# Kernel optimization log

Hardware: AMD Instinct MI355X
Metric: run time of the kernel (lower is better)

## Reference

```python
import jax, jax.numpy as jnp
import numpy as np

B, T, E, H = 8, 2048, 1024, 64

def setup_inputs() -> dict:
    key = jax.random.key(0)
    kx, kq, kk, kv = jax.random.split(key, 4)
    x = jax.random.normal(kx, (B, T, E), dtype=jnp.float32)
    # torch Linear(E, H, bias=False): weight [H, E]; store transposed [E, H]
    scale = 1.0 / np.sqrt(E)
    Wq = jax.random.uniform(kq, (E, H), dtype=jnp.float32, minval=-scale, maxval=scale)
    Wk = jax.random.uniform(kk, (E, H), dtype=jnp.float32, minval=-scale, maxval=scale)
    Wv = jax.random.uniform(kv, (E, H), dtype=jnp.float32, minval=-scale, maxval=scale)
    return {"x": x, "Wq": Wq, "Wk": Wk, "Wv": Wv}

def reference(x, Wq, Wk, Wv):
    # x: [B,T,E]
    q = x @ Wq  # [B,T,H]
    k = x @ Wk
    v = x @ Wv
    head_size = q.shape[-1]
    scores = jnp.einsum('bth,bsh->bts', q, k) * (head_size ** -0.5)  # [B,T,T]
    Tlen = x.shape[1]
    causal = jnp.tril(jnp.ones((Tlen, Tlen), dtype=bool))
    scores = jnp.where(causal, scores, -jnp.inf)
    weights = jax.nn.softmax(scores, axis=-1)
    # dropout p=0.0 -> identity
    out = jnp.einsum('bts,bsh->bth', weights, v)  # [B,T,H]
    return out
```

## Files before the change

kernel.cpp:

```cpp
#include <hip/hip_runtime.h>
#include <hip/hip_bf16.h>

#define B_  8
#define T_  2048
#define E_  1024
#define H_  64
#define BT_ (B_*T_)

typedef __attribute__((ext_vector_type(8))) __bf16 bf16x8;
typedef __attribute__((ext_vector_type(4))) float  f32x4;

__device__ __forceinline__ unsigned short f2bfu(float f) {
    union { float f; unsigned u; } v; v.f = f;
    unsigned r = v.u + 0x7fffu + ((v.u >> 16) & 1u);
    return (unsigned short)(r >> 16);
}

__device__ __forceinline__ unsigned pk2(float lo, float hi) {
    __hip_bfloat162 h = __float22bfloat162_rn(float2{lo, hi});
    union { __hip_bfloat162 h; unsigned u; } v; v.h = h;
    return v.u;
}

#define QSCALE (0.125f * 1.44269504f)

__global__ __launch_bounds__(256)
void wprep_kernel(const float* __restrict__ Wq,
                  const float* __restrict__ Wk,
                  const float* __restrict__ Wv,
                  unsigned short* __restrict__ wf)
{
    const int c = blockIdx.x / 3;
    const int m = blockIdx.x % 3;
    const float* W = (m == 0) ? Wq : (m == 1 ? Wk : Wv);
    const float scale = (m == 0) ? QSCALE : 1.0f;

    const int n    = threadIdx.x >> 6;
    const int lane = threadIdx.x & 63;
    const int quad = lane >> 4;
    const int col  = lane & 15;
    const int h    = n * 16 + col;

    unsigned short tmp[8];
#pragma unroll
    for (int j = 0; j < 8; ++j)
        tmp[j] = f2bfu(W[(c * 32 + quad * 8 + j) * H_ + h] * scale);
    *(uint4*)&wf[(((c * 3 + m) * 4 + n) * 64 + lane) * 8] = *(uint4*)tmp;
}

__global__ __launch_bounds__(256, 4)
void qkv_kernel(const float* __restrict__ x,
                const unsigned short* __restrict__ wf,
                unsigned short* __restrict__ qb,
                unsigned short* __restrict__ kb,
                unsigned short* __restrict__ vtb)
{
    const int tid  = threadIdx.x;
    const int wave = tid >> 6;
    const int lane = tid & 63;
    const int quad = lane >> 4;
    const int col  = lane & 15;
    const long r0  = (long)blockIdx.x * 16;

    f32x4 acc[3];
#pragma unroll
    for (int m = 0; m < 3; ++m) acc[m] = (f32x4){0.f, 0.f, 0.f, 0.f};

    const float* xb = x + (r0 + col) * E_ + quad * 8;

    float4 ax[4][2];
#pragma unroll
    for (int d = 0; d < 4; ++d) {
        ax[d][0] = *(const float4*)(xb + d * 32);
        ax[d][1] = *(const float4*)(xb + d * 32 + 4);
    }
    bf16x8 bw[2][3];
#pragma unroll
    for (int d = 0; d < 2; ++d)
#pragma unroll
        for (int m = 0; m < 3; ++m)
            bw[d][m] = *(const bf16x8*)&wf[(((d * 3 + m) * 4 + wave) * 64 + lane) * 8];

    for (int c = 0; c < 32; ++c) {
        float4 a0 = ax[c & 3][0], a1 = ax[c & 3][1];
        bf16x8 b0 = bw[c & 1][0], b1 = bw[c & 1][1], b2 = bw[c & 1][2];

        if (c + 4 < 32) {
            ax[c & 3][0] = *(const float4*)(xb + (c + 4) * 32);
            ax[c & 3][1] = *(const float4*)(xb + (c + 4) * 32 + 4);
        }
        if (c + 2 < 32) {
#pragma unroll
            for (int m = 0; m < 3; ++m)
                bw[c & 1][m] = *(const bf16x8*)&wf[((((c + 2) * 3 + m) * 4 + wave) * 64 + lane) * 8];
        }

        unsigned pk[4];
        pk[0] = pk2(a0.x, a0.y);
        pk[1] = pk2(a0.z, a0.w);
        pk[2] = pk2(a1.x, a1.y);
        pk[3] = pk2(a1.z, a1.w);
        bf16x8 af = *(bf16x8*)pk;

        acc[0] = __builtin_amdgcn_mfma_f32_16x16x32_bf16(af, b0, acc[0], 0, 0, 0);
        acc[1] = __builtin_amdgcn_mfma_f32_16x16x32_bf16(af, b1, acc[1], 0, 0, 0);
        acc[2] = __builtin_amdgcn_mfma_f32_16x16x32_bf16(af, b2, acc[2], 0, 0, 0);
    }

    const int bidx = (int)(r0 >> 11);
    const int h    = wave * 16 + col;
#pragma unroll
    for (int r = 0; r < 4; ++r) {
        long t = r0 + quad * 4 + r;
        qb[t * H_ + h] = f2bfu(acc[0][r]);
        kb[t * H_ + h] = f2bfu(acc[1][r]);
        vtb[((long)(bidx * H_ + h)) * T_ + (t & (T_ - 1))] = f2bfu(acc[2][r]);
    }
}

#define PSS 72

__global__ __launch_bounds__(512, 2)
void attn_kernel(const unsigned short* __restrict__ qb,
                 const unsigned short* __restrict__ kb,
                 const unsigned short* __restrict__ vtb,
                 float* __restrict__ out)
{
    __shared__ char smem[8 * 16 * 68 * 4 + 8 * 2 * 16 * 4];
    unsigned short* ps = (unsigned short*)smem;
    float* oc = (float*)smem;
    float* ml = (float*)(smem + 8 * 16 * 68 * 4);

    const int tid  = threadIdx.x;
    const int g    = tid >> 6;
    const int lane = tid & 63;
    const int quad = lane >> 4;
    const int col  = lane & 15;
    const int b    = blockIdx.x & 7;
    const int p    = blockIdx.x >> 3;

    const unsigned short* qbb = qb  + (long)b * T_ * H_;
    const unsigned short* kbb = kb  + (long)b * T_ * H_;
    const unsigned short* vbb = vtb + (long)b * H_ * T_;

    for (int half = 0; half < 2; ++half) {
        const int qt = half ? (127 - p) : p;
        const int nt = (qt + 4) >> 2;

        bf16x8 qa0 = *(const bf16x8*)&qbb[(qt * 16 + col) * H_ + quad * 8];
        bf16x8 qa1 = *(const bf16x8*)&qbb[(qt * 16 + col) * H_ + 32 + quad * 8];

        f32x4 o[4];
        float m_i[4], l_i[4];
#pragma unroll
        for (int n = 0; n < 4; ++n) o[n] = (f32x4){0.f, 0.f, 0.f, 0.f};
#pragma unroll
        for (int r = 0; r < 4; ++r) { m_i[r] = -1e30f; l_i[r] = 0.f; }

        bf16x8 kf[8];
        if (g < nt) {
#pragma unroll
            for (int kt = 0; kt < 4; ++kt) {
                const unsigned short* kp = kbb + ((long)(g * 64 + kt * 16 + col)) * H_ + quad * 8;
                kf[kt * 2]     = *(const bf16x8*)kp;
                kf[kt * 2 + 1] = *(const bf16x8*)(kp + 32);
            }
        }

        for (int s = g; s < nt; s += 8) {
            f32x4 sa[4];
#pragma unroll
            for (int kt = 0; kt < 4; ++kt) {
                sa[kt] = (f32x4){0.f, 0.f, 0.f, 0.f};
                sa[kt] = __builtin_amdgcn_mfma_f32_16x16x32_bf16(qa0, kf[kt * 2],     sa[kt], 0, 0, 0);
                sa[kt] = __builtin_amdgcn_mfma_f32_16x16x32_bf16(qa1, kf[kt * 2 + 1], sa[kt], 0, 0, 0);
            }

            if (s + 8 < nt) {
#pragma unroll
                for (int kt = 0; kt < 4; ++kt) {
                    const unsigned short* kp = kbb + ((long)((s + 8) * 64 + kt * 16 + col)) * H_ + quad * 8;
                    kf[kt * 2]     = *(const bf16x8*)kp;
                    kf[kt * 2 + 1] = *(const bf16x8*)(kp + 32);
                }
            }

            if (s == nt - 1) {
#pragma unroll
                for (int kt = 0; kt < 4; ++kt) {
                    int kg = s * 64 + kt * 16 + col;
#pragma unroll
                    for (int r = 0; r < 4; ++r) {
                        int qg = qt * 16 + quad * 4 + r;
                        if (kg > qg) sa[kt][r] = -1e30f;
                    }
                }
            }

            float mx[4];
#pragma unroll
            for (int r = 0; r < 4; ++r)
                mx[r] = fmaxf(fmaxf(sa[0][r], sa[1][r]), fmaxf(sa[2][r], sa[3][r]));
#pragma unroll
            for (int off = 1; off < 16; off <<= 1)
#pragma unroll
                for (int r = 0; r < 4; ++r)
                    mx[r] = fmaxf(mx[r], __shfl_xor(mx[r], off, 64));

            float alpha[4], mnew[4];
#pragma unroll
            for (int r = 0; r < 4; ++r) {
                mnew[r]  = fmaxf(m_i[r], mx[r]);
                alpha[r] = __builtin_amdgcn_exp2f(m_i[r] - mnew[r]);
                m_i[r]   = mnew[r];
            }

            float rs[4] = {0.f, 0.f, 0.f, 0.f};
#pragma unroll
            for (int kt = 0; kt < 4; ++kt)
#pragma unroll
                for (int r = 0; r < 4; ++r) {
                    float pv = __builtin_amdgcn_exp2f(sa[kt][r] - mnew[r]);
                    rs[r] += pv;
                    ps[g * 16 * PSS + (quad * 4 + r) * PSS + kt * 16 + col] = f2bfu(pv);
                }
#pragma unroll
            for (int off = 1; off < 16; off <<= 1)
#pragma unroll
                for (int r = 0; r < 4; ++r)
                    rs[r] += __shfl_xor(rs[r], off, 64);
#pragma unroll
            for (int r = 0; r < 4; ++r)
                l_i[r] = l_i[r] * alpha[r] + rs[r];

#pragma unroll
            for (int n = 0; n < 4; ++n)
#pragma unroll
                for (int r = 0; r < 4; ++r)
                    o[n][r] *= alpha[r];

            bf16x8 pa0 = *(const bf16x8*)&ps[g * 16 * PSS + col * PSS + quad * 8];
            bf16x8 pa1 = *(const bf16x8*)&ps[g * 16 * PSS + col * PSS + 32 + quad * 8];
#pragma unroll
            for (int n = 0; n < 4; ++n) {
                const unsigned short* vp = vbb + ((long)(n * 16 + col)) * T_ + s * 64 + quad * 8;
                bf16x8 vf0 = *(const bf16x8*)vp;
                bf16x8 vf1 = *(const bf16x8*)(vp + 32);
                o[n] = __builtin_amdgcn_mfma_f32_16x16x32_bf16(pa0, vf0, o[n], 0, 0, 0);
                o[n] = __builtin_amdgcn_mfma_f32_16x16x32_bf16(pa1, vf1, o[n], 0, 0, 0);
            }
        }

        __syncthreads();
#pragma unroll
        for (int r = 0; r < 4; ++r) {
            int row = quad * 4 + r;
#pragma unroll
            for (int n = 0; n < 4; ++n)
                oc[(g * 16 + row) * 68 + n * 16 + col] = o[n][r];
        }
        if (col == 0) {
#pragma unroll
            for (int r = 0; r < 4; ++r) {
                ml[(g * 2 + 0) * 16 + quad * 4 + r] = m_i[r];
                ml[(g * 2 + 1) * 16 + quad * 4 + r] = l_i[r];
            }
        }
        __syncthreads();

#pragma unroll
        for (int rr = 0; rr < 2; ++rr) {
            int row = g * 2 + rr;
            float M = ml[0 * 32 + row];
#pragma unroll
            for (int j = 1; j < 8; ++j) M = fmaxf(M, ml[j * 32 + row]);
            float lsum = 0.f, osum = 0.f;
#pragma unroll
            for (int j = 0; j < 8; ++j) {
                float wgt = __builtin_amdgcn_exp2f(ml[j * 32 + row] - M);
                lsum += ml[j * 32 + 16 + row] * wgt;
                osum += oc[(j * 16 + row) * 68 + lane] * wgt;
            }
            out[((long)b * T_ + qt * 16 + row) * H_ + lane] = osum / lsum;
        }
        __syncthreads();
    }
}

extern "C" void kernel_launch(void* const* d_in, const int* in_sizes, int n_in,
                              void* d_out, int out_size, void* d_ws, size_t ws_size,
                              hipStream_t stream) {
    (void)in_sizes; (void)n_in; (void)out_size; (void)ws_size;
    const float* x  = (const float*)d_in[0];
    const float* Wq = (const float*)d_in[1];
    const float* Wk = (const float*)d_in[2];
    const float* Wv = (const float*)d_in[3];

    unsigned short* qb  = (unsigned short*)d_ws;
    unsigned short* kb  = qb + (size_t)BT_ * H_;
    unsigned short* vtb = kb + (size_t)BT_ * H_;
    unsigned short* wf  = vtb + (size_t)BT_ * H_;

    wprep_kernel<<<96, 256, 0, stream>>>(Wq, Wk, Wv, wf);
    qkv_kernel<<<BT_ / 16, 256, 0, stream>>>(x, wf, qb, kb, vtb);
    attn_kernel<<<B_ * 64, 512, 0, stream>>>(qb, kb, vtb, (float*)d_out);
}
```

Before: 170.1 us.

## Stage QKV weights and x tiles in LDS and prefetch V tiles early

The QKV projection kernel now stages each chunk of packed weights in double-buffered shared memory, using global_load_lds DMA when the builtin is available. The x tile is converted to bf16 cooperatively into LDS, so each global element is loaded once per block instead of every wave reloading the weights. In the attention kernel, V tiles are loaded right after the QK MFMAs so their latency overlaps the softmax. The change adds a __syncthreads per K-chunk and extra LDS per block, which may reduce occupancy, and holding the V fragments raises register pressure.

New measurement: 159.6 us. 1.07x faster.

```diff
diff --git a/kernel.cpp b/kernel.cpp
--- a/kernel.cpp
+++ b/kernel.cpp
@@ -22,7 +22,25 @@
     return v.u;
 }
 
+#if defined(__has_builtin)
+#if __has_builtin(__builtin_amdgcn_global_load_lds)
+#define HAVE_GLL 1
+#endif
+#endif
+__device__ __forceinline__ void dma16(const void* g, void* lds_base, int lane) {
+#ifdef HAVE_GLL
+    __builtin_amdgcn_global_load_lds(
+        (const __attribute__((address_space(1))) unsigned*)(unsigned long long)g,
+        (__attribute__((address_space(3))) unsigned*)(unsigned)(unsigned long long)lds_base,
+        16, 0, 0);
+#else
+    *(uint4*)((char*)lds_base + lane * 16) = *(const uint4*)g;
+#endif
+}
+
 #define QSCALE (0.125f * 1.44269504f)
+
+#define WF_CHUNK_BYTES 12288
 
 __global__ __launch_bounds__(256)
 void wprep_kernel(const float* __restrict__ Wq,
@@ -55,8 +73,11 @@
                 unsigned short* __restrict__ kb,
                 unsigned short* __restrict__ vtb)
 {
+    __shared__ __align__(16) char           wfs[2][WF_CHUNK_BYTES];
+    __shared__ __align__(16) unsigned short xs[2][16 * 36];
+
     const int tid  = threadIdx.x;
-    const int wave = tid >> 6;
+    const int w    = tid >> 6;
     const int lane = tid & 63;
     const int quad = lane >> 4;
     const int col  = lane & 15;
@@ -66,49 +87,44 @@
 #pragma unroll
     for (int m = 0; m < 3; ++m) acc[m] = (f32x4){0.f, 0.f, 0.f, 0.f};
 
-    const float* xb = x + (r0 + col) * E_ + quad * 8;
-
-    float4 ax[4][2];
-#pragma unroll
-    for (int d = 0; d < 4; ++d) {
-        ax[d][0] = *(const float4*)(xb + d * 32);
-        ax[d][1] = *(const float4*)(xb + d * 32 + 4);
+    const char* wfb = (const char*)wf;
+    const int   row = tid >> 4;
+    const int   kk  = (tid & 15) * 2;
+    const float* xp = x + (r0 + row) * E_ + kk;
+
+    float2 xv = *(const float2*)xp;
+#pragma unroll
+    for (int j = 0; j < 3; ++j)
+        dma16(wfb + (w * 3 + j) * 1024 + lane * 16, &wfs[0][(w * 3 + j) * 1024], lane);
+    *(unsigned*)&xs[0][row * 36 + kk] = pk2(xv.x, xv.y);
+    xv = *(const float2*)(xp + 32);
+
+    for (int c = 0; c < 32; ++c) {
+        const int buf = c & 1;
+        __syncthreads();
+
+        if (c + 1 < 32) {
+#pragma unroll
+            for (int j = 0; j < 3; ++j)
+                dma16(wfb + (long)(c + 1) * WF_CHUNK_BYTES + (w * 3 + j) * 1024 + lane * 16,
+                      &wfs[buf ^ 1][(w * 3 + j) * 1024], lane);
+        }
+
+        bf16x8 af = *(const bf16x8*)&xs[buf][col * 36 + quad * 8];
+#pragma unroll
+        for (int m = 0; m < 3; ++m) {
+            bf16x8 bm = *(const bf16x8*)&wfs[buf][m * 4096 + w * 1024 + lane * 16];
+            acc[m] = __builtin_amdgcn_mfma_f32_16x16x32_bf16(af, bm, acc[m], 0, 0, 0);
+        }
+
+        if (c + 1 < 32) {
+            *(unsigned*)&xs[buf ^ 1][row * 36 + kk] = pk2(xv.x, xv.y);
+            if (c + 2 < 32) xv = *(const float2*)(xp + (c + 2) * 32);
+        }
     }
-    bf16x8 bw[2][3];
-#pragma unroll
-    for (int d = 0; d < 2; ++d)
-#pragma unroll
-        for (int m = 0; m < 3; ++m)
-            bw[d][m] = *(const bf16x8*)&wf[(((d * 3 + m) * 4 + wave) * 64 + lane) * 8];
-
-    for (int c = 0; c < 32; ++c) {
-        float4 a0 = ax[c & 3][0], a1 = ax[c & 3][1];
-        bf16x8 b0 = bw[c & 1][0], b1 = bw[c & 1][1], b2 = bw[c & 1][2];
-
-        if (c + 4 < 32) {
-            ax[c & 3][0] = *(const float4*)(xb + (c + 4) * 32);
-            ax[c & 3][1] = *(const float4*)(xb + (c + 4) * 32 + 4);
-        }
-        if (c + 2 < 32) {
-#pragma unroll
-            for (int m = 0; m < 3; ++m)
-                bw[c & 1][m] = *(const bf16x8*)&wf[((((c + 2) * 3 + m) * 4 + wave) * 64 + lane) * 8];
-        }
-
-        unsigned pk[4];
-        pk[0] = pk2(a0.x, a0.y);
-        pk[1] = pk2(a0.z, a0.w);
-        pk[2] = pk2(a1.x, a1.y);
-        pk[3] = pk2(a1.z, a1.w);
-        bf16x8 af = *(bf16x8*)pk;
-
-        acc[0] = __builtin_amdgcn_mfma_f32_16x16x32_bf16(af, b0, acc[0], 0, 0, 0);
-        acc[1] = __builtin_amdgcn_mfma_f32_16x16x32_bf16(af, b1, acc[1], 0, 0, 0);
-        acc[2] = __builtin_amdgcn_mfma_f32_16x16x32_bf16(af, b2, acc[2], 0, 0, 0);
-    }
 
     const int bidx = (int)(r0 >> 11);
-    const int h    = wave * 16 + col;
+    const int h    = w * 16 + col;
 #pragma unroll
     for (int r = 0; r < 4; ++r) {
         long t = r0 + quad * 4 + r;
@@ -176,6 +192,14 @@
                 sa[kt] = __builtin_amdgcn_mfma_f32_16x16x32_bf16(qa1, kf[kt * 2 + 1], sa[kt], 0, 0, 0);
             }
 
+            bf16x8 vf[8];
+#pragma unroll
+            for (int n = 0; n < 4; ++n) {
+                const unsigned short* vp = vbb + ((long)(n * 16 + col)) * T_ + s * 64 + quad * 8;
+                vf[n * 2]     = *(const bf16x8*)vp;
+                vf[n * 2 + 1] = *(const bf16x8*)(vp + 32);
+            }
+
             if (s + 8 < nt) {
 #pragma unroll
                 for (int kt = 0; kt < 4; ++kt) {
@@ -243,11 +267,8 @@
             bf16x8 pa1 = *(const bf16x8*)&ps[g * 16 * PSS + col * PSS + 32 + quad * 8];
 #pragma unroll
             for (int n = 0; n < 4; ++n) {
-                const unsigned short* vp = vbb + ((long)(n * 16 + col)) * T_ + s * 64 + quad * 8;
-                bf16x8 vf0 = *(const bf16x8*)vp;
-                bf16x8 vf1 = *(const bf16x8*)(vp + 32);
-                o[n] = __builtin_amdgcn_mfma_f32_16x16x32_bf16(pa0, vf0, o[n], 0, 0, 0);
-                o[n] = __builtin_amdgcn_mfma_f32_16x16x32_bf16(pa1, vf1, o[n], 0, 0, 0);
+                o[n] = __builtin_amdgcn_mfma_f32_16x16x32_bf16(pa0, vf[n * 2],     o[n], 0, 0, 0);
+                o[n] = __builtin_amdgcn_mfma_f32_16x16x32_bf16(pa1, vf[n * 2 + 1], o[n], 0, 0, 0);
             }
         }
 
```
